# Kernel tuning notes

Measured on AMD Instinct MI355X. Metric: run time of the kernel, lower is better.

Reference implementation:

```python
import jax, jax.numpy as jnp
import numpy as np

N_NODES = 50000
IN_DIM = 256
OUT_DIM = 128
NNZ_FEAT = 800000
NNZ_ADJ = 800000


def setup_inputs() -> dict:
    key = jax.random.key(0)
    ks = jax.random.split(key, 10)
    inp = {
        "feat_row": jax.random.randint(ks[0], (NNZ_FEAT,), 0, N_NODES, dtype=jnp.int32),
        "feat_col": jax.random.randint(ks[1], (NNZ_FEAT,), 0, IN_DIM, dtype=jnp.int32),
        "feat_vals": jnp.ones((NNZ_FEAT,), dtype=jnp.float32),  # binary features (int-cast in original)
        "adj1_row": jax.random.randint(ks[2], (NNZ_ADJ,), 0, N_NODES, dtype=jnp.int32),
        "adj1_col": jax.random.randint(ks[3], (NNZ_ADJ,), 0, N_NODES, dtype=jnp.int32),
        "adj1_vals": jax.random.uniform(ks[4], (NNZ_ADJ,), dtype=jnp.float32),
        "adj2_row": jax.random.randint(ks[5], (NNZ_ADJ,), 0, N_NODES, dtype=jnp.int32),
        "adj2_col": jax.random.randint(ks[6], (NNZ_ADJ,), 0, N_NODES, dtype=jnp.int32),
        "adj2_vals": jax.random.uniform(ks[7], (NNZ_ADJ,), dtype=jnp.float32),
    }
    # Glorot-uniform weights as in weight_variable_glorot
    lim = np.sqrt(6.0 / (IN_DIM + OUT_DIM))
    inp["W1"] = jax.random.uniform(ks[8], (IN_DIM, OUT_DIM), minval=-lim, maxval=lim, dtype=jnp.float32)
    inp["W2"] = jax.random.uniform(ks[9], (IN_DIM, OUT_DIM), minval=-lim, maxval=lim, dtype=jnp.float32)
    inp["n_nodes"] = N_NODES
    return inp


def _spmm_feat(row, col, vals, W, n_nodes):
    # X (sparse [N, F]) @ W ([F, D]) -> [N, D]
    msg = vals[:, None] * W[col]  # [nnz, D]
    return jax.ops.segment_sum(msg, row, num_segments=n_nodes)


def _spmm_adj(row, col, vals, H, n_nodes):
    # A (sparse [N, N]) @ H ([N, D]) -> [N, D]
    msg = vals[:, None] * H[col]  # [E, D]
    return jax.ops.segment_sum(msg, row, num_segments=n_nodes)


def reference(feat_row, feat_col, feat_vals, adj1_row, adj1_col, adj1_vals,
              adj2_row, adj2_col, adj2_vals, W1, W2, n_nodes):
    # dropout=0.0 -> keep_prob=1 -> sparse dropout is identity with scale 1.0
    xw1 = _spmm_feat(feat_row, feat_col, feat_vals, W1, n_nodes)   # [N, D]
    x1 = _spmm_adj(adj1_row, adj1_col, adj1_vals, xw1, n_nodes)    # [N, D]
    xw2 = _spmm_feat(feat_row, feat_col, feat_vals, W2, n_nodes)
    x2 = _spmm_adj(adj2_row, adj2_col, adj2_vals, xw2, n_nodes)
    return jax.nn.relu(x1 + x2)
```

## Files before the change

### kernel.cpp

```cpp
#include <hip/hip_runtime.h>
#include <hip/hip_fp16.h>

#define N_NODES 50000
#define IN_DIM 256
#define OUT_DIM 128
#define NNZ 800000
#define SCAN_N (3 * N_NODES)
#define TOTAL_NNZ (3 * NNZ)

#define NSB 511
#define SUBW 98
#define SUBCAP 6144

#define EB 1024
#define SB_GRID ((NNZ + EB - 1) / EB)

#define ADJ_SL 4
#define ADJ_RC ((N_NODES + 63) / 64)

typedef float vf4 __attribute__((ext_vector_type(4)));

static __device__ __forceinline__ unsigned pack_cv(int c, float v) {
    return ((unsigned)c << 16) | (unsigned)__half_as_ushort(__float2half(v));
}
static __device__ __forceinline__ int   upk_c(unsigned pk) { return (int)(pk >> 16); }
static __device__ __forceinline__ float upk_v(unsigned pk) {
    return __half2float(__ushort_as_half((unsigned short)(pk & 0xffffu)));
}
static __device__ __forceinline__ float h2f(unsigned short h) {
    return __half2float(__ushort_as_half(h));
}
static __device__ __forceinline__ unsigned pk2h(float x, float y) {
    return (unsigned)__half_as_ushort(__float2half(x))
         | ((unsigned)__half_as_ushort(__float2half(y)) << 16);
}

__global__ void wprep_kernel(const float* __restrict__ W1,
                             const float* __restrict__ W2,
                             uint4* __restrict__ Wc) {
    int idx = blockIdx.x * 256 + threadIdx.x;
    const float4* w1 = (const float4*)W1;
    const float4* w2 = (const float4*)W2;
    float4 a = w1[idx];
    float4 b = w2[idx];
    uint4 o;
    o.x = pk2h(a.x, a.y);
    o.y = pk2h(a.z, a.w);
    o.z = pk2h(b.x, b.y);
    o.w = pk2h(b.z, b.w);
    Wc[idx] = o;
}

__global__ __launch_bounds__(512) void superbucket_kernel(
        const int* __restrict__ fr, const int* __restrict__ fc,
        const float* __restrict__ fv,
        const int* __restrict__ a1r, const int* __restrict__ a1c,
        const float* __restrict__ a1v,
        const int* __restrict__ a2r, const int* __restrict__ a2c,
        const float* __restrict__ a2v,
        int* __restrict__ subcur,
        unsigned* __restrict__ gpack2,
        unsigned short* __restrict__ gmeta2) {
    __shared__ unsigned long long stage[3 * EB];
    __shared__ int c512[512];
    __shared__ int offE[512];
    __shared__ int gb[512];
    int t = threadIdx.x;
    c512[t] = 0;
    __syncthreads();
    int base = blockIdx.x * EB;
    int nE = NNZ - base; if (nE > EB) nE = EB;
    int tot = 3 * nE;

    unsigned long long ent[6]; int sbA[6]; int loc[6];
#pragma unroll
    for (int k = 0; k < 2; ++k) {
        int i = k * 512 + t;
        int e = base + i;
        if (i < nE) {
            int r0 = __builtin_nontemporal_load(&fr[e]);
            unsigned p0 = pack_cv(__builtin_nontemporal_load(&fc[e]),
                                  __builtin_nontemporal_load(&fv[e]));
            int s0 = r0 / SUBW;
            ent[3*k]   = ((unsigned long long)s0 << 48)
                       | ((unsigned long long)(r0 - s0 * SUBW) << 32) | p0;
            sbA[3*k] = s0;  loc[3*k] = atomicAdd(&c512[s0], 1);

            int r1 = __builtin_nontemporal_load(&a1r[e]);
            unsigned p1 = pack_cv(__builtin_nontemporal_load(&a1c[e]),
                                  __builtin_nontemporal_load(&a1v[e]));
            int s1 = r1 / SUBW;
            ent[3*k+1] = ((unsigned long long)s1 << 48)
                       | ((unsigned long long)(SUBW + r1 - s1 * SUBW) << 32) | p1;
            sbA[3*k+1] = s1;  loc[3*k+1] = atomicAdd(&c512[s1], 1);

            int r2 = __builtin_nontemporal_load(&a2r[e]);
            unsigned p2 = pack_cv(__builtin_nontemporal_load(&a2c[e]),
                                  __builtin_nontemporal_load(&a2v[e]));
            int s2 = r2 / SUBW;
            ent[3*k+2] = ((unsigned long long)s2 << 48)
                       | ((unsigned long long)(2 * SUBW + r2 - s2 * SUBW) << 32) | p2;
            sbA[3*k+2] = s2;  loc[3*k+2] = atomicAdd(&c512[s2], 1);
        } else {
            sbA[3*k] = sbA[3*k+1] = sbA[3*k+2] = -1;
        }
    }
    __syncthreads();
    offE[t] = c512[t];
    __syncthreads();
    for (int off = 1; off < 512; off <<= 1) {
        int v = (t >= off) ? offE[t - off] : 0;
        __syncthreads();
        offE[t] += v;
        __syncthreads();
    }
    int excl = offE[t] - c512[t];
    __syncthreads();
    offE[t] = excl;
    if (c512[t] > 0) gb[t] = atomicAdd(&subcur[t], c512[t]);
    __syncthreads();
#pragma unroll
    for (int k = 0; k < 6; ++k) {
        if (sbA[k] >= 0) stage[offE[sbA[k]] + loc[k]] = ent[k];
    }
    __syncthreads();
    for (int i = t; i < tot; i += 512) {
        unsigned long long v = stage[i];
        int sb = (int)(v >> 48);
        int g = sb * SUBCAP + gb[sb] + (i - offE[sb]);
        gpack2[g] = (unsigned)v;
        gmeta2[g] = (unsigned short)(v >> 32);
    }
}

__global__ __launch_bounds__(512) void sort_write_kernel(
        const unsigned* __restrict__ gpack2,
        const unsigned short* __restrict__ gmeta2,
        const int* __restrict__ subcur,
        int* __restrict__ cur3,
        int* __restrict__ starts,
        int* __restrict__ rowlen,
        unsigned* __restrict__ spack) {
    int sb = blockIdx.x;
    int n = subcur[sb];
    __shared__ int h[512];
    __shared__ int e[512];
    __shared__ int cur[512];
    __shared__ int segbase[4];
    __shared__ int gbs[3];
    __shared__ unsigned sorted[SUBCAP];
    int t = threadIdx.x;
    h[t] = 0;
    __syncthreads();
    long base = (long)sb * SUBCAP;
    unsigned pk[12]; short ky[12];
#pragma unroll
    for (int k = 0; k < 12; ++k) {
        int i = t + k * 512;
        if (i < n) {
            pk[k] = gpack2[base + i];
            ky[k] = (short)gmeta2[base + i];
            atomicAdd(&h[ky[k]], 1);
        } else ky[k] = -1;
    }
    __syncthreads();
    e[t] = h[t];
    __syncthreads();
    for (int off = 1; off < 512; off <<= 1) {
        int v = (t >= off) ? e[t - off] : 0;
        __syncthreads();
        e[t] += v;
        __syncthreads();
    }
    int excl = e[t] - h[t];
    __syncthreads();
    e[t] = excl;
    cur[t] = excl;
    __syncthreads();
    if (t == 0) {
        segbase[0] = 0;
        segbase[1] = e[SUBW];
        segbase[2] = e[2 * SUBW];
        segbase[3] = n;
    }
    __syncthreads();
    if (t < 3) gbs[t] = atomicAdd(&cur3[t], segbase[t + 1] - segbase[t]);
#pragma unroll
    for (int k = 0; k < 12; ++k) {
        if (ky[k] >= 0) {
            int pos = atomicAdd(&cur[ky[k]], 1);
            sorted[pos] = pk[k];
        }
    }
    __syncthreads();
    if (t < 3 * SUBW) {
        int s = t / SUBW, d = t - s * SUBW;
        int r = sb * SUBW + d;
        if (r < N_NODES) {
            int gr = s * N_NODES + r;
            starts[gr] = s * NNZ + gbs[s] + (e[t] - segbase[s]);
            rowlen[gr] = h[t];
        }
    }
    int s1 = segbase[1], s2 = segbase[2];
#pragma unroll
    for (int k = 0; k < 12; ++k) {
        int i = t + k * 512;
        if (i < n) {
            int sg = (i < s1) ? 0 : ((i < s2) ? 1 : 2);
            spack[sg * NNZ + gbs[sg] + (i - segbase[sg])] = sorted[i];
        }
    }
}

__global__ void feat_gather_kernel(const int* __restrict__ starts,
                                   const int* __restrict__ rowlen,
                                   const unsigned* __restrict__ spack,
                                   const uint4* __restrict__ Wc,
                                   ushort4* __restrict__ xw1s,
                                   ushort4* __restrict__ xw2s) {
    int lane = threadIdx.x & 31;
    int sub  = threadIdx.x >> 5;
    int r = blockIdx.x * 8 + sub;
    if (r >= N_NODES) return;
    int s = starts[r];
    int e = s + rowlen[r];
    float4 a1 = make_float4(0.f, 0.f, 0.f, 0.f);
    float4 a2 = make_float4(0.f, 0.f, 0.f, 0.f);
    for (int base = s; base < e; base += 32) {
        int n = e - base;
        int m = (n < 32) ? n : 32;
        unsigned pk = (lane < m) ? spack[base + lane] : 0u;
        int j = 0;
        for (; j + 7 < m; j += 8) {
            unsigned pp[8]; uint4 wv[8];
#pragma unroll
            for (int k = 0; k < 8; ++k) pp[k] = __shfl(pk, j + k, 32);
#pragma unroll
            for (int k = 0; k < 8; ++k) wv[k] = Wc[upk_c(pp[k]) * 32 + lane];
#pragma unroll
            for (int k = 0; k < 8; ++k) {
                float v = upk_v(pp[k]);
                a1.x += v * h2f((unsigned short)(wv[k].x & 0xffffu));
                a1.y += v * h2f((unsigned short)(wv[k].x >> 16));
                a1.z += v * h2f((unsigned short)(wv[k].y & 0xffffu));
                a1.w += v * h2f((unsigned short)(wv[k].y >> 16));
                a2.x += v * h2f((unsigned short)(wv[k].z & 0xffffu));
                a2.y += v * h2f((unsigned short)(wv[k].z >> 16));
                a2.z += v * h2f((unsigned short)(wv[k].w & 0xffffu));
                a2.w += v * h2f((unsigned short)(wv[k].w >> 16));
            }
        }
        for (; j < m; ++j) {
            unsigned pj = __shfl(pk, j, 32);
            float v = upk_v(pj);
            uint4 wv = Wc[upk_c(pj) * 32 + lane];
            a1.x += v * h2f((unsigned short)(wv.x & 0xffffu));
            a1.y += v * h2f((unsigned short)(wv.x >> 16));
            a1.z += v * h2f((unsigned short)(wv.y & 0xffffu));
            a1.w += v * h2f((unsigned short)(wv.y >> 16));
            a2.x += v * h2f((unsigned short)(wv.z & 0xffffu));
            a2.y += v * h2f((unsigned short)(wv.z >> 16));
            a2.z += v * h2f((unsigned short)(wv.w & 0xffffu));
            a2.w += v * h2f((unsigned short)(wv.w >> 16));
        }
    }
    ushort4 q1, q2;
    q1.x = __half_as_ushort(__float2half(a1.x)); q1.y = __half_as_ushort(__float2half(a1.y));
    q1.z = __half_as_ushort(__float2half(a1.z)); q1.w = __half_as_ushort(__float2half(a1.w));
    q2.x = __half_as_ushort(__float2half(a2.x)); q2.y = __half_as_ushort(__float2half(a2.y));
    q2.z = __half_as_ushort(__float2half(a2.z)); q2.w = __half_as_ushort(__float2half(a2.w));
    size_t idx = (size_t)(lane >> 3) * (N_NODES * 8) + (size_t)r * 8 + (lane & 7);
    xw1s[idx] = q1;
    xw2s[idx] = q2;
}

__global__ __launch_bounds__(512) void adj_pass_fused(
        const int* __restrict__ starts,
        const int* __restrict__ rowlen,
        const unsigned* __restrict__ spack,
        const ushort4* __restrict__ xw1s,
        const ushort4* __restrict__ xw2s,
        vf4* __restrict__ out) {
    int s  = blockIdx.x & (ADJ_SL - 1);
    int rc = blockIdx.x >> 2;
    int g  = threadIdx.x >> 3;
    int q  = threadIdx.x & 7;
    int r  = rc * 64 + g;
    bool valid = (r < N_NODES);
    vf4 acc = {0.f, 0.f, 0.f, 0.f};

#pragma unroll
    for (int rel = 0; rel < 2; ++rel) {
        const ushort4* __restrict__ sl =
            ((rel == 0) ? xw1s : xw2s) + (size_t)s * (N_NODES * 8);
        int st = 0, en = 0;
        if (valid) {
            st = starts[(1 + rel) * N_NODES + r];
            en = st + rowlen[(1 + rel) * N_NODES + r];
        }
        for (int base = st; base < en; base += 16) {
            int m = en - base;
            unsigned pk0 = (q < m)     ? spack[base + q]     : 0u;
            unsigned pk1 = (8 + q < m) ? spack[base + 8 + q] : 0u;
            {
                unsigned pp[8]; ushort4 xx[8];
#pragma unroll
                for (int k = 0; k < 8; ++k) pp[k] = __shfl(pk0, k, 8);
#pragma unroll
                for (int k = 0; k < 8; ++k) xx[k] = sl[upk_c(pp[k]) * 8 + q];
#pragma unroll
                for (int k = 0; k < 8; ++k) {
                    float v = upk_v(pp[k]);
                    acc.x += v * h2f(xx[k].x); acc.y += v * h2f(xx[k].y);
                    acc.z += v * h2f(xx[k].z); acc.w += v * h2f(xx[k].w);
                }
            }
            if (m <= 8) continue;
            {
                unsigned pp[8]; ushort4 xx[8];
#pragma unroll
                for (int k = 0; k < 8; ++k) pp[k] = __shfl(pk1, k, 8);
#pragma unroll
                for (int k = 0; k < 8; ++k) xx[k] = sl[upk_c(pp[k]) * 8 + q];
#pragma unroll
                for (int k = 0; k < 8; ++k) {
                    float v = upk_v(pp[k]);
                    acc.x += v * h2f(xx[k].x); acc.y += v * h2f(xx[k].y);
                    acc.z += v * h2f(xx[k].z); acc.w += v * h2f(xx[k].w);
                }
            }
        }
    }
    if (valid) {
        vf4 res;
        res.x = fmaxf(acc.x, 0.f);
        res.y = fmaxf(acc.y, 0.f);
        res.z = fmaxf(acc.z, 0.f);
        res.w = fmaxf(acc.w, 0.f);
        __builtin_nontemporal_store(res, &out[(size_t)r * 32 + s * 8 + q]);
    }
}

extern "C" void kernel_launch(void* const* d_in, const int* in_sizes, int n_in,
                              void* d_out, int out_size, void* d_ws, size_t ws_size,
                              hipStream_t stream) {
    const int*   feat_row  = (const int*)  d_in[0];
    const int*   feat_col  = (const int*)  d_in[1];
    const float* feat_vals = (const float*)d_in[2];
    const int*   adj1_row  = (const int*)  d_in[3];
    const int*   adj1_col  = (const int*)  d_in[4];
    const float* adj1_vals = (const float*)d_in[5];
    const int*   adj2_row  = (const int*)  d_in[6];
    const int*   adj2_col  = (const int*)  d_in[7];
    const float* adj2_vals = (const float*)d_in[8];
    const float* W1        = (const float*)d_in[9];
    const float* W2        = (const float*)d_in[10];

    char* ws = (char*)d_ws;
    unsigned* spack = (unsigned*)ws;            ws += (size_t)TOTAL_NNZ * 4;
    int*      starts= (int*)ws;                 ws += (size_t)SCAN_N * 4;
    int*      rowlen= (int*)ws;                 ws += (size_t)SCAN_N * 4;
    int*      subcur= (int*)ws;                 ws += 512 * 4;
    int*      cur3  = (int*)ws;                 ws += 16 * 4;
    uint4*    Wc    = (uint4*)ws;               ws += (size_t)256 * 32 * 16;
    char*     bkt   = ws;
    unsigned* gpack2 = (unsigned*)bkt;
    unsigned short* gmeta2 = (unsigned short*)(bkt + (size_t)NSB * SUBCAP * 4);
    ushort4*  xw1s  = (ushort4*)bkt;
    ushort4*  xw2s  = (ushort4*)(bkt + (size_t)N_NODES * OUT_DIM * 2);

    (void)hipMemsetAsync(subcur, 0, (512 + 16) * sizeof(int), stream);

    wprep_kernel<<<32, 256, 0, stream>>>(W1, W2, Wc);

    superbucket_kernel<<<SB_GRID, 512, 0, stream>>>(
        feat_row, feat_col, feat_vals,
        adj1_row, adj1_col, adj1_vals,
        adj2_row, adj2_col, adj2_vals,
        subcur, gpack2, gmeta2);

    sort_write_kernel<<<NSB, 512, 0, stream>>>(
        gpack2, gmeta2, subcur, cur3, starts, rowlen, spack);

    const int grid_rows = N_NODES / 8;
    feat_gather_kernel<<<grid_rows, 256, 0, stream>>>(
        starts, rowlen, spack, Wc, xw1s, xw2s);

    adj_pass_fused<<<ADJ_SL * ADJ_RC, 512, 0, stream>>>(
        starts, rowlen, spack, xw1s, xw2s, (vf4*)d_out);
}
```

Baseline: 223.8 us.

## Fuse feature gather into sort kernel, reading sorted feature entries from LDS

The feature-side SpMM (X·W1, X·W2) now runs inside the sort-write kernel, straight from the per-superbucket sorted array in shared memory. The separate feature gather kernel, the global write of the feature segment of spack and its re-read all go away. The cost is that the sort kernel gets more work on only 511 blocks, so parallelism is lower than the old 6250-block gather. The workspace is also un-aliased so gpack2/gmeta2 and xw1s/xw2s no longer overlap.

```diff
diff --git a/kernel.cpp b/kernel.cpp
--- a/kernel.cpp
+++ b/kernel.cpp
@@ -133,14 +133,17 @@
     }
 }
 
-__global__ __launch_bounds__(512) void sort_write_kernel(
+__global__ __launch_bounds__(512) void sort_write_feat_kernel(
         const unsigned* __restrict__ gpack2,
         const unsigned short* __restrict__ gmeta2,
         const int* __restrict__ subcur,
         int* __restrict__ cur3,
         int* __restrict__ starts,
         int* __restrict__ rowlen,
-        unsigned* __restrict__ spack) {
+        unsigned* __restrict__ spack,
+        const uint4* __restrict__ Wc,
+        ushort4* __restrict__ xw1s,
+        ushort4* __restrict__ xw2s) {
     int sb = blockIdx.x;
     int n = subcur[sb];
     __shared__ int h[512];
@@ -206,73 +209,90 @@
 #pragma unroll
     for (int k = 0; k < 12; ++k) {
         int i = t + k * 512;
-        if (i < n) {
-            int sg = (i < s1) ? 0 : ((i < s2) ? 1 : 2);
+        if (i >= s1 && i < n) {
+            int sg = (i < s2) ? 1 : 2;
             spack[sg * NNZ + gbs[sg] + (i - segbase[sg])] = sorted[i];
         }
     }
-}
-
-__global__ void feat_gather_kernel(const int* __restrict__ starts,
-                                   const int* __restrict__ rowlen,
-                                   const unsigned* __restrict__ spack,
-                                   const uint4* __restrict__ Wc,
-                                   ushort4* __restrict__ xw1s,
-                                   ushort4* __restrict__ xw2s) {
-    int lane = threadIdx.x & 31;
-    int sub  = threadIdx.x >> 5;
-    int r = blockIdx.x * 8 + sub;
-    if (r >= N_NODES) return;
-    int s = starts[r];
-    int e = s + rowlen[r];
-    float4 a1 = make_float4(0.f, 0.f, 0.f, 0.f);
-    float4 a2 = make_float4(0.f, 0.f, 0.f, 0.f);
-    for (int base = s; base < e; base += 32) {
-        int n = e - base;
-        int m = (n < 32) ? n : 32;
-        unsigned pk = (lane < m) ? spack[base + lane] : 0u;
+    int grp  = t >> 5;
+    int lane = t & 31;
+    for (int rowIdx = grp; rowIdx < SUBW; rowIdx += 16) {
+        int r = sb * SUBW + rowIdx;
+        if (r >= N_NODES) continue;
+        int cnt = h[rowIdx];
+        int bs  = e[rowIdx];
+        float4 a1 = make_float4(0.f, 0.f, 0.f, 0.f);
+        float4 a2 = make_float4(0.f, 0.f, 0.f, 0.f);
         int j = 0;
-        for (; j + 7 < m; j += 8) {
-            unsigned pp[8]; uint4 wv[8];
-#pragma unroll
-            for (int k = 0; k < 8; ++k) pp[k] = __shfl(pk, j + k, 32);
-#pragma unroll
-            for (int k = 0; k < 8; ++k) wv[k] = Wc[upk_c(pp[k]) * 32 + lane];
-#pragma unroll
-            for (int k = 0; k < 8; ++k) {
-                float v = upk_v(pp[k]);
-                a1.x += v * h2f((unsigned short)(wv[k].x & 0xffffu));
-                a1.y += v * h2f((unsigned short)(wv[k].x >> 16));
-                a1.z += v * h2f((unsigned short)(wv[k].y & 0xffffu));
-                a1.w += v * h2f((unsigned short)(wv[k].y >> 16));
-                a2.x += v * h2f((unsigned short)(wv[k].z & 0xffffu));
-                a2.y += v * h2f((unsigned short)(wv[k].z >> 16));
-                a2.z += v * h2f((unsigned short)(wv[k].w & 0xffffu));
-                a2.w += v * h2f((unsigned short)(wv[k].w >> 16));
-            }
-        }
-        for (; j < m; ++j) {
-            unsigned pj = __shfl(pk, j, 32);
-            float v = upk_v(pj);
-            uint4 wv = Wc[upk_c(pj) * 32 + lane];
-            a1.x += v * h2f((unsigned short)(wv.x & 0xffffu));
-            a1.y += v * h2f((unsigned short)(wv.x >> 16));
-            a1.z += v * h2f((unsigned short)(wv.y & 0xffffu));
-            a1.w += v * h2f((unsigned short)(wv.y >> 16));
-            a2.x += v * h2f((unsigned short)(wv.z & 0xffffu));
-            a2.y += v * h2f((unsigned short)(wv.z >> 16));
-            a2.z += v * h2f((unsigned short)(wv.w & 0xffffu));
-            a2.w += v * h2f((unsigned short)(wv.w >> 16));
-        }
-    }
-    ushort4 q1, q2;
-    q1.x = __half_as_ushort(__float2half(a1.x)); q1.y = __half_as_ushort(__float2half(a1.y));
-    q1.z = __half_as_ushort(__float2half(a1.z)); q1.w = __half_as_ushort(__float2half(a1.w));
-    q2.x = __half_as_ushort(__float2half(a2.x)); q2.y = __half_as_ushort(__float2half(a2.y));
-    q2.z = __half_as_ushort(__float2half(a2.z)); q2.w = __half_as_ushort(__float2half(a2.w));
-    size_t idx = (size_t)(lane >> 3) * (N_NODES * 8) + (size_t)r * 8 + (lane & 7);
-    xw1s[idx] = q1;
-    xw2s[idx] = q2;
+        for (; j + 3 < cnt; j += 4) {
+            unsigned p0 = sorted[bs + j];
+            unsigned p1 = sorted[bs + j + 1];
+            unsigned p2 = sorted[bs + j + 2];
+            unsigned p3 = sorted[bs + j + 3];
+            uint4 w0 = Wc[upk_c(p0) * 32 + lane];
+            uint4 w1 = Wc[upk_c(p1) * 32 + lane];
+            uint4 w2 = Wc[upk_c(p2) * 32 + lane];
+            uint4 w3 = Wc[upk_c(p3) * 32 + lane];
+            float v0 = upk_v(p0), v1 = upk_v(p1), v2 = upk_v(p2), v3 = upk_v(p3);
+            a1.x += v0 * h2f((unsigned short)(w0.x & 0xffffu));
+            a1.y += v0 * h2f((unsigned short)(w0.x >> 16));
+            a1.z += v0 * h2f((unsigned short)(w0.y & 0xffffu));
+            a1.w += v0 * h2f((unsigned short)(w0.y >> 16));
+            a2.x += v0 * h2f((unsigned short)(w0.z & 0xffffu));
+            a2.y += v0 * h2f((unsigned short)(w0.z >> 16));
+            a2.z += v0 * h2f((unsigned short)(w0.w & 0xffffu));
+            a2.w += v0 * h2f((unsigned short)(w0.w >> 16));
+            a1.x += v1 * h2f((unsigned short)(w1.x & 0xffffu));
+            a1.y += v1 * h2f((unsigned short)(w1.x >> 16));
+            a1.z += v1 * h2f((unsigned short)(w1.y & 0xffffu));
+            a1.w += v1 * h2f((unsigned short)(w1.y >> 16));
+            a2.x += v1 * h2f((unsigned short)(w1.z & 0xffffu));
+            a2.y += v1 * h2f((unsigned short)(w1.z >> 16));
+            a2.z += v1 * h2f((unsigned short)(w1.w & 0xffffu));
+            a2.w += v1 * h2f((unsigned short)(w1.w >> 16));
+            a1.x += v2 * h2f((unsigned short)(w2.x & 0xffffu));
+            a1.y += v2 * h2f((unsigned short)(w2.x >> 16));
+            a1.z += v2 * h2f((unsigned short)(w2.y & 0xffffu));
+            a1.w += v2 * h2f((unsigned short)(w2.y >> 16));
+            a2.x += v2 * h2f((unsigned short)(w2.z & 0xffffu));
+            a2.y += v2 * h2f((unsigned short)(w2.z >> 16));
+            a2.z += v2 * h2f((unsigned short)(w2.w & 0xffffu));
+            a2.w += v2 * h2f((unsigned short)(w2.w >> 16));
+            a1.x += v3 * h2f((unsigned short)(w3.x & 0xffffu));
+            a1.y += v3 * h2f((unsigned short)(w3.x >> 16));
+            a1.z += v3 * h2f((unsigned short)(w3.y & 0xffffu));
+            a1.w += v3 * h2f((unsigned short)(w3.y >> 16));
+            a2.x += v3 * h2f((unsigned short)(w3.z & 0xffffu));
+            a2.y += v3 * h2f((unsigned short)(w3.z >> 16));
+            a2.z += v3 * h2f((unsigned short)(w3.w & 0xffffu));
+            a2.w += v3 * h2f((unsigned short)(w3.w >> 16));
+        }
+        for (; j < cnt; ++j) {
+            unsigned p = sorted[bs + j];
+            float v = upk_v(p);
+            uint4 w = Wc[upk_c(p) * 32 + lane];
+            a1.x += v * h2f((unsigned short)(w.x & 0xffffu));
+            a1.y += v * h2f((unsigned short)(w.x >> 16));
+            a1.z += v * h2f((unsigned short)(w.y & 0xffffu));
+            a1.w += v * h2f((unsigned short)(w.y >> 16));
+            a2.x += v * h2f((unsigned short)(w.z & 0xffffu));
+            a2.y += v * h2f((unsigned short)(w.z >> 16));
+            a2.z += v * h2f((unsigned short)(w.w & 0xffffu));
+            a2.w += v * h2f((unsigned short)(w.w >> 16));
+        }
+        ushort4 q1, q2;
+        q1.x = __half_as_ushort(__float2half(a1.x));
+        q1.y = __half_as_ushort(__float2half(a1.y));
+        q1.z = __half_as_ushort(__float2half(a1.z));
+        q1.w = __half_as_ushort(__float2half(a1.w));
+        q2.x = __half_as_ushort(__float2half(a2.x));
+        q2.y = __half_as_ushort(__float2half(a2.y));
+        q2.z = __half_as_ushort(__float2half(a2.z));
+        q2.w = __half_as_ushort(__float2half(a2.w));
+        size_t idx = (size_t)(lane >> 3) * (N_NODES * 8) + (size_t)r * 8 + (lane & 7);
+        xw1s[idx] = q1;
+        xw2s[idx] = q2;
+    }
 }
 
 __global__ __launch_bounds__(512) void adj_pass_fused(
@@ -364,11 +384,10 @@
     int*      subcur= (int*)ws;                 ws += 512 * 4;
     int*      cur3  = (int*)ws;                 ws += 16 * 4;
     uint4*    Wc    = (uint4*)ws;               ws += (size_t)256 * 32 * 16;
-    char*     bkt   = ws;
-    unsigned* gpack2 = (unsigned*)bkt;
-    unsigned short* gmeta2 = (unsigned short*)(bkt + (size_t)NSB * SUBCAP * 4);
-    ushort4*  xw1s  = (ushort4*)bkt;
-    ushort4*  xw2s  = (ushort4*)(bkt + (size_t)N_NODES * OUT_DIM * 2);
+    unsigned* gpack2 = (unsigned*)ws;           ws += (size_t)NSB * SUBCAP * 4;
+    unsigned short* gmeta2 = (unsigned short*)ws; ws += (size_t)NSB * SUBCAP * 2;
+    ushort4*  xw1s  = (ushort4*)ws;             ws += (size_t)N_NODES * OUT_DIM * 2;
+    ushort4*  xw2s  = (ushort4*)ws;             ws += (size_t)N_NODES * OUT_DIM * 2;
 
     (void)hipMemsetAsync(subcur, 0, (512 + 16) * sizeof(int), stream);
 
@@ -380,12 +399,8 @@
         adj2_row, adj2_col, adj2_vals,
         subcur, gpack2, gmeta2);
 
-    sort_write_kernel<<<NSB, 512, 0, stream>>>(
-        gpack2, gmeta2, subcur, cur3, starts, rowlen, spack);
-
-    const int grid_rows = N_NODES / 8;
-    feat_gather_kernel<<<grid_rows, 256, 0, stream>>>(
-        starts, rowlen, spack, Wc, xw1s, xw2s);
+    sort_write_feat_kernel<<<NSB, 512, 0, stream>>>(
+        gpack2, gmeta2, subcur, cur3, starts, rowlen, spack, Wc, xw1s, xw2s);
 
     adj_pass_fused<<<ADJ_SL * ADJ_RC, 512, 0, stream>>>(
         starts, rowlen, spack, xw1s, xw2s, (vf4*)d_out);
```

New measurement: 219.2 us. 1.02x faster.
